# Kernel optimization log

Measured on AMD Instinct MI355X. Metric: run time of the kernel, lower is better.

The kernel has to match this reference:

```python
import jax, jax.numpy as jnp
import numpy as np

EPS = 0.001
FLOW_WARP_WEIGHT = 1.0
_GRAY_W = jnp.array([0.299, 0.587, 0.114], dtype=jnp.float32)


def _to_gray(img):
    # img: [B, 3, H, W] -> [B, 1, H, W] luminance
    return jnp.einsum('bchw,c->bhw', img, _GRAY_W.astype(img.dtype))[:, None]


def _resize_bilinear_align_corners(x, h_out, w_out):
    # x: [B, C, H, W] -> [B, C, h_out, w_out], bilinear, align_corners=True
    B, C, H, W = x.shape
    sy = jnp.arange(h_out, dtype=x.dtype) * ((H - 1) / max(h_out - 1, 1))
    sx = jnp.arange(w_out, dtype=x.dtype) * ((W - 1) / max(w_out - 1, 1))
    y0 = jnp.floor(sy).astype(jnp.int32)
    x0 = jnp.floor(sx).astype(jnp.int32)
    y1 = jnp.minimum(y0 + 1, H - 1)
    x1 = jnp.minimum(x0 + 1, W - 1)
    wy = (sy - y0)[:, None]            # [h_out, 1]
    wx = (sx - x0)[None, :]            # [1, w_out]
    # interp along H
    xh = x[:, :, y0, :] * (1.0 - wy)[..., None].squeeze(-1)[None, None] if False else x[:, :, y0, :] * (1.0 - wy) + x[:, :, y1, :] * wy  # [B,C,h_out,W]
    # interp along W
    out = xh[:, :, :, x0] * (1.0 - wx) + xh[:, :, :, x1] * wx
    return out


def _resize_flow_to_image(flow, h_img, w_img):
    flow_uv = flow[:, :2]
    fh, fw = flow_uv.shape[-2:]
    if (fh, fw) == (h_img, w_img):
        return flow_uv
    r = _resize_bilinear_align_corners(flow_uv, h_img, w_img)
    scale = jnp.array([w_img / max(fw, 1), h_img / max(fh, 1)], dtype=flow.dtype)
    return r * scale[None, :, None, None]


def _bilinear_sample_zeros(img, gx, gy):
    # img: [B, 1, H, W]; gx, gy: [B, H, W] pixel coords (align_corners=True)
    B, _, H, W = img.shape
    x0f = jnp.floor(gx)
    y0f = jnp.floor(gy)
    wx = gx - x0f
    wy = gy - y0f
    x0 = x0f.astype(jnp.int32)
    y0 = y0f.astype(jnp.int32)
    b = jnp.arange(B)[:, None, None]

    def gather(yi, xi):
        valid = (xi >= 0) & (xi <= W - 1) & (yi >= 0) & (yi <= H - 1)
        v = img[b, 0, jnp.clip(yi, 0, H - 1), jnp.clip(xi, 0, W - 1)]
        return jnp.where(valid, v, jnp.zeros((), img.dtype))

    v00 = gather(y0, x0)
    v01 = gather(y0, x0 + 1)
    v10 = gather(y0 + 1, x0)
    v11 = gather(y0 + 1, x0 + 1)
    out = (v00 * (1 - wx) * (1 - wy) + v01 * wx * (1 - wy)
           + v10 * (1 - wx) * wy + v11 * wx * wy)
    return out[:, None]  # [B,1,H,W]


def _forward(pred_prev, pred_next, flow_prev_to_next):
    prev_g = _to_gray(pred_prev)   # [B,1,H,W]
    next_g = _to_gray(pred_next)
    B, _, H, W = prev_g.shape
    flow_uv = _resize_flow_to_image(flow_prev_to_next, H, W)  # [B,2,H,W]
    yy, xx = jnp.meshgrid(jnp.arange(H, dtype=prev_g.dtype),
                          jnp.arange(W, dtype=prev_g.dtype), indexing='ij')
    gx = xx[None] + flow_uv[:, 0]  # [B,H,W]
    gy = yy[None] + flow_uv[:, 1]
    valid = ((gx >= 0) & (gx <= W - 1) & (gy >= 0) & (gy <= H - 1)).astype(prev_g.dtype)
    warped = _bilinear_sample_zeros(next_g, gx, gy)  # [B,1,H,W]
    diff = prev_g - warped
    valid_mask = valid[:, None]
    valid_count = jnp.maximum(valid_mask.sum(), 1.0)
    loss_map = jnp.sqrt(diff * diff + EPS * EPS) * valid_mask
    loss = loss_map.sum() / valid_count
    return FLOW_WARP_WEIGHT * loss, loss


def setup_inputs() -> dict:
    key = jax.random.key(0)
    k1, k2, k3 = jax.random.split(key, 3)
    pred_prev = jax.random.uniform(k1, (16, 3, 512, 512), dtype=jnp.float32)
    pred_next = jax.random.uniform(k2, (16, 3, 512, 512), dtype=jnp.float32)
    flow = jax.random.normal(k3, (16, 2, 128, 128), dtype=jnp.float32)
    return {"pred_prev": pred_prev, "pred_next": pred_next, "flow_prev_to_next": flow}


def reference(pred_prev, pred_next, flow_prev_to_next):
    return _forward(pred_prev, pred_next, flow_prev_to_next)
```

## Files before the change

### kernel.cpp

```cpp
#include <hip/hip_runtime.h>


typedef _Float16 half8 __attribute__((ext_vector_type(8)));

constexpr int B  = 16;
constexpr int H  = 512;
constexpr int W  = 512;
constexpr int FH = 128;
constexpr int FW = 128;
constexpr int HW  = H * W;
constexpr int IMG = 3 * HW;
constexpr int FHW = FH * FW;
constexpr float EPS = 0.001f;

constexpr int P    = 32;
constexpr int PW   = W + 2 * P;
constexpr int PH   = H + 2 * P;
constexpr int PIMG = PW * PH;
constexpr int PQ8  = PH * (PW / 8);

constexpr int TX = 64, TY = 32;
constexpr int TW = 120, TH = 80;
constexpr int FROWS  = 10;
constexpr int FLOW_F = 2 * FROWS * FW;

constexpr int NB = 2048;

__global__ __launch_bounds__(256) void pad_gray_kernel(
    const float* __restrict__ nxt, _Float16* __restrict__ g)
{
    const int q  = blockIdx.x * 256 + threadIdx.x;
    const int b  = q / PQ8;
    const int r  = q - b * PQ8;
    const int py = r / (PW / 8);
    const int qx = r - py * (PW / 8);
    const int y  = py - P;
    const int xs = qx * 8 - P;
    half8 o = (half8)0;
    if ((unsigned)y < (unsigned)H && (unsigned)xs <= (unsigned)(W - 8)) {
        const float* __restrict__ nb = nxt + (long)b * IMG + y * W + xs;
        #pragma unroll
        for (int h = 0; h < 2; ++h) {
            const float4 rr = *(const float4*)(nb + 4 * h);
            const float4 gg = *(const float4*)(nb + HW + 4 * h);
            const float4 bl = *(const float4*)(nb + 2 * HW + 4 * h);
            o[4 * h + 0] = (_Float16)(0.299f * rr.x + 0.587f * gg.x + 0.114f * bl.x);
            o[4 * h + 1] = (_Float16)(0.299f * rr.y + 0.587f * gg.y + 0.114f * bl.y);
            o[4 * h + 2] = (_Float16)(0.299f * rr.z + 0.587f * gg.z + 0.114f * bl.z);
            o[4 * h + 3] = (_Float16)(0.299f * rr.w + 0.587f * gg.w + 0.114f * bl.w);
        }
    }
    *(half8*)(g + (long)b * PIMG + py * PW + qx * 8) = o;
}

__global__ __launch_bounds__(256) void loss_kernel(
    const float* __restrict__ prev, const _Float16* __restrict__ gpad,
    const float* __restrict__ flow, double* __restrict__ psum,
    unsigned int* __restrict__ pcnt)
{
    __shared__ __align__(16) _Float16 smh[TW * TH];
    __shared__ __align__(16) float    smf[FLOW_F];

    const int bid = ((blockIdx.x & 7) << 8) | (blockIdx.x >> 3);
    const int b   = bid >> 7;
    const int t   = bid & 127;
    const int tx  = t & 7;
    const int ty  = t >> 3;
    const int x0t = tx * TX;
    const int y0t = ty * TY;

    const float fr = (float)(127.0 / 511.0);
    const int fy_lo = (int)((float)y0t * fr);

    const _Float16* __restrict__ gb = gpad + (long)b * PIMG;

    {
        const _Float16* __restrict__ src = gb + (y0t + 8) * PW + (x0t + 8);
        for (int it = threadIdx.x; it < TH * (TW / 8); it += 256) {
            const int r = it / (TW / 8), c = it - r * (TW / 8);
            *(uint4*)(smh + r * TW + c * 8) = *(const uint4*)(src + r * PW + c * 8);
        }
        const float* __restrict__ fsrc = flow + (long)b * 2 * FHW;
        for (int it = threadIdx.x; it < 2 * FROWS * (FW / 4); it += 256) {
            const int c    = it / (FROWS * (FW / 4));
            const int rr   = (it - c * (FROWS * (FW / 4))) >> 5;
            const int c4   = it & 31;
            const int frow = min(fy_lo + rr, FH - 1);
            const float4 v = *(const float4*)(fsrc + c * FHW + frow * FW + c4 * 4);
            *(float4*)(smf + c * (FROWS * FW) + rr * FW + c4 * 4) = v;
        }
    }

    const int xq = threadIdx.x & 15;
    const int yl = threadIdx.x >> 4;
    const int xb = x0t + xq * 4;

    float pg[2][4];
    #pragma unroll
    for (int k = 0; k < 2; ++k) {
        const int y = y0t + yl + k * 16;
        const float* __restrict__ pb = prev + (long)b * IMG + y * W + xb;
        const float4 pr  = *(const float4*)(pb);
        const float4 pgc = *(const float4*)(pb + HW);
        const float4 plc = *(const float4*)(pb + 2 * HW);
        pg[k][0] = 0.299f * pr.x + 0.587f * pgc.x + 0.114f * plc.x;
        pg[k][1] = 0.299f * pr.y + 0.587f * pgc.y + 0.114f * plc.y;
        pg[k][2] = 0.299f * pr.z + 0.587f * pgc.z + 0.114f * plc.z;
        pg[k][3] = 0.299f * pr.w + 0.587f * pgc.w + 0.114f * plc.w;
    }

    __syncthreads();

    const float sxfb = (float)xb * fr;
    const int F  = (int)sxfb;
    const int F2 = min(F + 2, FW - 1);

    double lsum = 0.0;
    unsigned int lcnt = 0;

    #pragma unroll
    for (int k = 0; k < 2; ++k) {
        const int y = y0t + yl + k * 16;

        const float syf = (float)y * fr;
        const int   fy0 = (int)syf;
        const float wy  = syf - (float)fy0;
        const int r0 = fy0 - fy_lo;
        const int r1 = min(fy0 + 1, FH - 1) - fy_lo;

        const float* __restrict__ su = smf;
        const float* __restrict__ sv = smf + FROWS * FW;
        const float u0a = su[r0 * FW + F], u0b = su[r0 * FW + F + 1], u0c = su[r0 * FW + F2];
        const float u1a = su[r1 * FW + F], u1b = su[r1 * FW + F + 1], u1c = su[r1 * FW + F2];
        const float v0a = sv[r0 * FW + F], v0b = sv[r0 * FW + F + 1], v0c = sv[r0 * FW + F2];
        const float v1a = sv[r1 * FW + F], v1b = sv[r1 * FW + F + 1], v1c = sv[r1 * FW + F2];

        #pragma unroll
        for (int i = 0; i < 4; ++i) {
            const int x = xb + i;
            const float sxf = (float)x * fr;
            const int   fx0 = (int)sxf;
            const float wx  = sxf - (float)fx0;
            const int   d   = fx0 - F;

            const float u00 = d ? u0b : u0a, u01 = d ? u0c : u0b;
            const float u10 = d ? u1b : u1a, u11 = d ? u1c : u1b;
            const float v00 = d ? v0b : v0a, v01 = d ? v0c : v0b;
            const float v10 = d ? v1b : v1a, v11 = d ? v1c : v1b;

            const float uc0 = u00 * (1.0f - wy) + u10 * wy;
            const float uc1 = u01 * (1.0f - wy) + u11 * wy;
            const float vc0 = v00 * (1.0f - wy) + v10 * wy;
            const float vc1 = v01 * (1.0f - wy) + v11 * wy;
            const float u = (uc0 * (1.0f - wx) + uc1 * wx) * 4.0f;
            const float v = (vc0 * (1.0f - wx) + vc1 * wx) * 4.0f;

            const float gx = (float)x + u;
            const float gy = (float)y + v;
            const float vm = ((gx >= 0.0f) & (gx <= (float)(W - 1)) &
                              (gy >= 0.0f) & (gy <= (float)(H - 1))) ? 1.0f : 0.0f;

            const float gxf = floorf(gx), gyf = floorf(gy);
            const float wwx = gx - gxf,  wwy = gy - gyf;
            const int ix0 = (int)gxf, iy0 = (int)gyf;

            const int cx = ix0 - (x0t - 24);
            const int ry = iy0 - (y0t - 24);
            float c00, c01, c10, c11;
            if ((unsigned)cx <= (unsigned)(TW - 2) && (unsigned)ry <= (unsigned)(TH - 2)) {
                const int la = ry * TW + cx;
                c00 = (float)smh[la];      c01 = (float)smh[la + 1];
                c10 = (float)smh[la + TW]; c11 = (float)smh[la + TW + 1];
            } else {
                const int iyc = min(max(iy0, -P), PH - P - 2);
                const int ixc = min(max(ix0, -P), PW - P - 2);
                const _Float16* __restrict__ gp = gb + (iyc + P) * PW + (ixc + P);
                c00 = (float)gp[0];  c01 = (float)gp[1];
                c10 = (float)gp[PW]; c11 = (float)gp[PW + 1];
            }

            const float warped = c00 * (1.0f - wwx) * (1.0f - wwy)
                               + c01 * wwx * (1.0f - wwy)
                               + c10 * (1.0f - wwx) * wwy
                               + c11 * wwx * wwy;
            const float diff = pg[k][i] - warped;
            const float l = sqrtf(diff * diff + EPS * EPS);
            lsum += (double)(l * vm);
            lcnt += (unsigned int)vm;
        }
    }

    #pragma unroll
    for (int off = 32; off > 0; off >>= 1) {
        lsum += __shfl_down(lsum, off);
        lcnt += __shfl_down(lcnt, off);
    }
    __shared__ double s_sum[4];
    __shared__ unsigned int s_cnt[4];
    const int wid = threadIdx.x >> 6, lane = threadIdx.x & 63;
    if (lane == 0) { s_sum[wid] = lsum; s_cnt[wid] = lcnt; }
    __syncthreads();
    if (threadIdx.x == 0) {
        psum[blockIdx.x] = s_sum[0] + s_sum[1] + s_sum[2] + s_sum[3];
        pcnt[blockIdx.x] = s_cnt[0] + s_cnt[1] + s_cnt[2] + s_cnt[3];
    }
}

__global__ __launch_bounds__(256) void reduce_kernel(
    const double* __restrict__ psum, const unsigned int* __restrict__ pcnt,
    int nb, float* __restrict__ out)
{
    double s = 0.0;
    unsigned long long c = 0;
    for (int i = threadIdx.x; i < nb; i += 256) {
        s += psum[i];
        c += (unsigned long long)pcnt[i];
    }
    #pragma unroll
    for (int off = 32; off > 0; off >>= 1) {
        s += __shfl_down(s, off);
        c += __shfl_down(c, off);
    }
    __shared__ double ss[4];
    __shared__ unsigned long long sc[4];
    const int wid = threadIdx.x >> 6, lane = threadIdx.x & 63;
    if (lane == 0) { ss[wid] = s; sc[wid] = c; }
    __syncthreads();
    if (threadIdx.x == 0) {
        double ts = ss[0] + ss[1] + ss[2] + ss[3];
        double tc = (double)(sc[0] + sc[1] + sc[2] + sc[3]);
        if (tc < 1.0) tc = 1.0;
        const float loss = (float)(ts / tc);
        out[0] = loss;
        out[1] = loss;
    }
}

__device__ __forceinline__ float gray3(const float* __restrict__ img, int off) {
    return 0.299f * img[off] + 0.587f * img[HW + off] + 0.114f * img[2 * HW + off];
}

__global__ __launch_bounds__(256) void flow_loss_mono_kernel(
    const float* __restrict__ prev, const float* __restrict__ nxt,
    const float* __restrict__ flow, double* __restrict__ psum,
    unsigned int* __restrict__ pcnt)
{
    const int nquad = B * HW / 4;
    const float fr = (float)(127.0 / 511.0);
    double lsum = 0.0;
    unsigned int lcnt = 0;
    for (int q = blockIdx.x * blockDim.x + threadIdx.x; q < nquad;
         q += gridDim.x * blockDim.x) {
        const int pix = q * 4;
        const int b   = pix >> 18;
        const int rem = pix & (HW - 1);
        const int y   = rem >> 9;
        const int x0  = rem & 511;
        const float* __restrict__ pb = prev + (long)b * IMG;
        const float* __restrict__ nb = nxt  + (long)b * IMG;
        const float* __restrict__ fu = flow + (long)b * 2 * FHW;
        const float* __restrict__ fv = fu + FHW;
        const float syf = (float)y * fr;
        const int   fy0 = (int)syf;
        const int   fy1 = min(fy0 + 1, FH - 1);
        const float wy  = syf - (float)fy0;
        #pragma unroll
        for (int i = 0; i < 4; ++i) {
            const int x = x0 + i;
            const float sxf = (float)x * fr;
            const int   fx0 = (int)sxf;
            const int   fx1 = min(fx0 + 1, FW - 1);
            const float wx  = sxf - (float)fx0;
            const float uc0 = fu[fy0 * FW + fx0] * (1.0f - wy) + fu[fy1 * FW + fx0] * wy;
            const float uc1 = fu[fy0 * FW + fx1] * (1.0f - wy) + fu[fy1 * FW + fx1] * wy;
            const float vc0 = fv[fy0 * FW + fx0] * (1.0f - wy) + fv[fy1 * FW + fx0] * wy;
            const float vc1 = fv[fy0 * FW + fx1] * (1.0f - wy) + fv[fy1 * FW + fx1] * wy;
            const float u = (uc0 * (1.0f - wx) + uc1 * wx) * 4.0f;
            const float v = (vc0 * (1.0f - wx) + vc1 * wx) * 4.0f;
            const float gx = (float)x + u;
            const float gy = (float)y + v;
            const float vm = ((gx >= 0.0f) & (gx <= (float)(W - 1)) &
                              (gy >= 0.0f) & (gy <= (float)(H - 1))) ? 1.0f : 0.0f;
            const float gxf = floorf(gx), gyf = floorf(gy);
            const float wwx = gx - gxf, wwy = gy - gyf;
            const int ix0 = (int)gxf, iy0 = (int)gyf;
            const int xc0 = min(max(ix0, 0), W - 1), xc1 = min(max(ix0 + 1, 0), W - 1);
            const int yc0 = min(max(iy0, 0), H - 1), yc1 = min(max(iy0 + 1, 0), H - 1);
            const float okx0 = (ix0 >= 0 && ix0 < W) ? 1.f : 0.f;
            const float okx1 = (ix0 + 1 >= 0 && ix0 + 1 < W) ? 1.f : 0.f;
            const float oky0 = (iy0 >= 0 && iy0 < H) ? 1.f : 0.f;
            const float oky1 = (iy0 + 1 >= 0 && iy0 + 1 < H) ? 1.f : 0.f;
            const float c00 = gray3(nb, yc0 * W + xc0) * oky0 * okx0;
            const float c01 = gray3(nb, yc0 * W + xc1) * oky0 * okx1;
            const float c10 = gray3(nb, yc1 * W + xc0) * oky1 * okx0;
            const float c11 = gray3(nb, yc1 * W + xc1) * oky1 * okx1;
            const float warped = c00 * (1.0f - wwx) * (1.0f - wwy)
                               + c01 * wwx * (1.0f - wwy)
                               + c10 * (1.0f - wwx) * wwy
                               + c11 * wwx * wwy;
            const float pgv = gray3(pb, y * W + x);
            const float diff = pgv - warped;
            const float l = sqrtf(diff * diff + EPS * EPS);
            lsum += (double)(l * vm);
            lcnt += (unsigned int)vm;
        }
    }
    #pragma unroll
    for (int off = 32; off > 0; off >>= 1) {
        lsum += __shfl_down(lsum, off);
        lcnt += __shfl_down(lcnt, off);
    }
    __shared__ double s_sum[4];
    __shared__ unsigned int s_cnt[4];
    const int wid = threadIdx.x >> 6, lane = threadIdx.x & 63;
    if (lane == 0) { s_sum[wid] = lsum; s_cnt[wid] = lcnt; }
    __syncthreads();
    if (threadIdx.x == 0) {
        psum[blockIdx.x] = s_sum[0] + s_sum[1] + s_sum[2] + s_sum[3];
        pcnt[blockIdx.x] = s_cnt[0] + s_cnt[1] + s_cnt[2] + s_cnt[3];
    }
}

extern "C" void kernel_launch(void* const* d_in, const int* in_sizes, int n_in,
                              void* d_out, int out_size, void* d_ws, size_t ws_size,
                              hipStream_t stream) {
    const float* prev = (const float*)d_in[0];
    const float* nxt  = (const float*)d_in[1];
    const float* flow = (const float*)d_in[2];
    float* out = (float*)d_out;

    double* psum = (double*)d_ws;
    unsigned int* pcnt = (unsigned int*)((char*)d_ws + NB * 8);
    const size_t gbuf_off = ((size_t)NB * 12 + 4095) & ~(size_t)4095;
    const size_t pad_bytes = (size_t)B * PIMG * sizeof(_Float16);

    if (ws_size >= gbuf_off + pad_bytes) {
        _Float16* gbuf = (_Float16*)((char*)d_ws + gbuf_off);
        pad_gray_kernel<<<dim3(B * PQ8 / 256), dim3(256), 0, stream>>>(nxt, gbuf);
        loss_kernel<<<dim3(NB), dim3(256), 0, stream>>>(
            prev, gbuf, flow, psum, pcnt);
        reduce_kernel<<<dim3(1), dim3(256), 0, stream>>>(psum, pcnt, NB, out);
    } else {
        flow_loss_mono_kernel<<<dim3(2048), dim3(256), 0, stream>>>(
            prev, nxt, flow, psum, pcnt);
        reduce_kernel<<<dim3(1), dim3(256), 0, stream>>>(psum, pcnt, 2048, out);
    }
}
```

Baseline: 36.67 us.

## Fuse grayscale conversion into loss kernel tile load, drop padded gray buffer

Removes the separate pad_gray kernel and its fp16 padded intermediate. Each loss block now converts its halo tile of the next frame from RGB fp32 to fp16 gray directly into shared memory, and falls back to on-the-fly gray from global memory for out-of-tile samples. This saves a kernel launch and the intermediate write/read. The cost is redundant RGB reads across overlapping halos, three times the bytes per pixel. The workspace-size fallback path is also removed.

Result: slower. 44.02 us (+20.0%).

```diff
diff --git a/kernel.cpp b/kernel.cpp
--- a/kernel.cpp
+++ b/kernel.cpp
@@ -1,7 +1,7 @@
 #include <hip/hip_runtime.h>
 
 
-typedef _Float16 half8 __attribute__((ext_vector_type(8)));
+typedef _Float16 half4v __attribute__((ext_vector_type(4)));
 
 constexpr int B  = 16;
 constexpr int H  = 512;
@@ -13,12 +13,6 @@
 constexpr int FHW = FH * FW;
 constexpr float EPS = 0.001f;
 
-constexpr int P    = 32;
-constexpr int PW   = W + 2 * P;
-constexpr int PH   = H + 2 * P;
-constexpr int PIMG = PW * PH;
-constexpr int PQ8  = PH * (PW / 8);
-
 constexpr int TX = 64, TY = 32;
 constexpr int TW = 120, TH = 80;
 constexpr int FROWS  = 10;
@@ -26,35 +20,12 @@
 
 constexpr int NB = 2048;
 
-__global__ __launch_bounds__(256) void pad_gray_kernel(
-    const float* __restrict__ nxt, _Float16* __restrict__ g)
-{
-    const int q  = blockIdx.x * 256 + threadIdx.x;
-    const int b  = q / PQ8;
-    const int r  = q - b * PQ8;
-    const int py = r / (PW / 8);
-    const int qx = r - py * (PW / 8);
-    const int y  = py - P;
-    const int xs = qx * 8 - P;
-    half8 o = (half8)0;
-    if ((unsigned)y < (unsigned)H && (unsigned)xs <= (unsigned)(W - 8)) {
-        const float* __restrict__ nb = nxt + (long)b * IMG + y * W + xs;
-        #pragma unroll
-        for (int h = 0; h < 2; ++h) {
-            const float4 rr = *(const float4*)(nb + 4 * h);
-            const float4 gg = *(const float4*)(nb + HW + 4 * h);
-            const float4 bl = *(const float4*)(nb + 2 * HW + 4 * h);
-            o[4 * h + 0] = (_Float16)(0.299f * rr.x + 0.587f * gg.x + 0.114f * bl.x);
-            o[4 * h + 1] = (_Float16)(0.299f * rr.y + 0.587f * gg.y + 0.114f * bl.y);
-            o[4 * h + 2] = (_Float16)(0.299f * rr.z + 0.587f * gg.z + 0.114f * bl.z);
-            o[4 * h + 3] = (_Float16)(0.299f * rr.w + 0.587f * gg.w + 0.114f * bl.w);
-        }
-    }
-    *(half8*)(g + (long)b * PIMG + py * PW + qx * 8) = o;
+__device__ __forceinline__ float gray3(const float* __restrict__ img, int off) {
+    return 0.299f * img[off] + 0.587f * img[HW + off] + 0.114f * img[2 * HW + off];
 }
 
 __global__ __launch_bounds__(256) void loss_kernel(
-    const float* __restrict__ prev, const _Float16* __restrict__ gpad,
+    const float* __restrict__ prev, const float* __restrict__ nxt,
     const float* __restrict__ flow, double* __restrict__ psum,
     unsigned int* __restrict__ pcnt)
 {
@@ -72,14 +43,26 @@
     const float fr = (float)(127.0 / 511.0);
     const int fy_lo = (int)((float)y0t * fr);
 
-    const _Float16* __restrict__ gb = gpad + (long)b * PIMG;
-
+    const float* __restrict__ nb = nxt + (long)b * IMG;
+
+    for (int it = threadIdx.x; it < TH * (TW / 4); it += 256) {
+        const int r  = it / (TW / 4), c = it - r * (TW / 4);
+        const int sy = y0t - 24 + r;
+        const int sx = x0t - 24 + c * 4;
+        half4v hv = (half4v)0;
+        if ((unsigned)sy < (unsigned)H && (unsigned)sx <= (unsigned)(W - 4)) {
+            const float* __restrict__ p = nb + sy * W + sx;
+            const float4 rr = *(const float4*)(p);
+            const float4 gg = *(const float4*)(p + HW);
+            const float4 bl = *(const float4*)(p + 2 * HW);
+            hv[0] = (_Float16)(0.299f * rr.x + 0.587f * gg.x + 0.114f * bl.x);
+            hv[1] = (_Float16)(0.299f * rr.y + 0.587f * gg.y + 0.114f * bl.y);
+            hv[2] = (_Float16)(0.299f * rr.z + 0.587f * gg.z + 0.114f * bl.z);
+            hv[3] = (_Float16)(0.299f * rr.w + 0.587f * gg.w + 0.114f * bl.w);
+        }
+        *(half4v*)(smh + r * TW + c * 4) = hv;
+    }
     {
-        const _Float16* __restrict__ src = gb + (y0t + 8) * PW + (x0t + 8);
-        for (int it = threadIdx.x; it < TH * (TW / 8); it += 256) {
-            const int r = it / (TW / 8), c = it - r * (TW / 8);
-            *(uint4*)(smh + r * TW + c * 8) = *(const uint4*)(src + r * PW + c * 8);
-        }
         const float* __restrict__ fsrc = flow + (long)b * 2 * FHW;
         for (int it = threadIdx.x; it < 2 * FROWS * (FW / 4); it += 256) {
             const int c    = it / (FROWS * (FW / 4));
@@ -172,11 +155,16 @@
                 c00 = (float)smh[la];      c01 = (float)smh[la + 1];
                 c10 = (float)smh[la + TW]; c11 = (float)smh[la + TW + 1];
             } else {
-                const int iyc = min(max(iy0, -P), PH - P - 2);
-                const int ixc = min(max(ix0, -P), PW - P - 2);
-                const _Float16* __restrict__ gp = gb + (iyc + P) * PW + (ixc + P);
-                c00 = (float)gp[0];  c01 = (float)gp[1];
-                c10 = (float)gp[PW]; c11 = (float)gp[PW + 1];
+                const bool vx0g = (ix0 >= 0) & (ix0 < W);
+                const bool vx1g = (ix0 + 1 >= 0) & (ix0 + 1 < W);
+                const bool vy0g = (iy0 >= 0) & (iy0 < H);
+                const bool vy1g = (iy0 + 1 >= 0) & (iy0 + 1 < H);
+                const int xc0 = min(max(ix0, 0), W - 1), xc1 = min(max(ix0 + 1, 0), W - 1);
+                const int yc0 = min(max(iy0, 0), H - 1), yc1 = min(max(iy0 + 1, 0), H - 1);
+                c00 = (vy0g & vx0g) ? gray3(nb, yc0 * W + xc0) : 0.0f;
+                c01 = (vy0g & vx1g) ? gray3(nb, yc0 * W + xc1) : 0.0f;
+                c10 = (vy1g & vx0g) ? gray3(nb, yc1 * W + xc0) : 0.0f;
+                c11 = (vy1g & vx1g) ? gray3(nb, yc1 * W + xc1) : 0.0f;
             }
 
             const float warped = c00 * (1.0f - wwx) * (1.0f - wwy)
@@ -236,91 +224,6 @@
     }
 }
 
-__device__ __forceinline__ float gray3(const float* __restrict__ img, int off) {
-    return 0.299f * img[off] + 0.587f * img[HW + off] + 0.114f * img[2 * HW + off];
-}
-
-__global__ __launch_bounds__(256) void flow_loss_mono_kernel(
-    const float* __restrict__ prev, const float* __restrict__ nxt,
-    const float* __restrict__ flow, double* __restrict__ psum,
-    unsigned int* __restrict__ pcnt)
-{
-    const int nquad = B * HW / 4;
-    const float fr = (float)(127.0 / 511.0);
-    double lsum = 0.0;
-    unsigned int lcnt = 0;
-    for (int q = blockIdx.x * blockDim.x + threadIdx.x; q < nquad;
-         q += gridDim.x * blockDim.x) {
-        const int pix = q * 4;
-        const int b   = pix >> 18;
-        const int rem = pix & (HW - 1);
-        const int y   = rem >> 9;
-        const int x0  = rem & 511;
-        const float* __restrict__ pb = prev + (long)b * IMG;
-        const float* __restrict__ nb = nxt  + (long)b * IMG;
-        const float* __restrict__ fu = flow + (long)b * 2 * FHW;
-        const float* __restrict__ fv = fu + FHW;
-        const float syf = (float)y * fr;
-        const int   fy0 = (int)syf;
-        const int   fy1 = min(fy0 + 1, FH - 1);
-        const float wy  = syf - (float)fy0;
-        #pragma unroll
-        for (int i = 0; i < 4; ++i) {
-            const int x = x0 + i;
-            const float sxf = (float)x * fr;
-            const int   fx0 = (int)sxf;
-            const int   fx1 = min(fx0 + 1, FW - 1);
-            const float wx  = sxf - (float)fx0;
-            const float uc0 = fu[fy0 * FW + fx0] * (1.0f - wy) + fu[fy1 * FW + fx0] * wy;
-            const float uc1 = fu[fy0 * FW + fx1] * (1.0f - wy) + fu[fy1 * FW + fx1] * wy;
-            const float vc0 = fv[fy0 * FW + fx0] * (1.0f - wy) + fv[fy1 * FW + fx0] * wy;
-            const float vc1 = fv[fy0 * FW + fx1] * (1.0f - wy) + fv[fy1 * FW + fx1] * wy;
-            const float u = (uc0 * (1.0f - wx) + uc1 * wx) * 4.0f;
-            const float v = (vc0 * (1.0f - wx) + vc1 * wx) * 4.0f;
-            const float gx = (float)x + u;
-            const float gy = (float)y + v;
-            const float vm = ((gx >= 0.0f) & (gx <= (float)(W - 1)) &
-                              (gy >= 0.0f) & (gy <= (float)(H - 1))) ? 1.0f : 0.0f;
-            const float gxf = floorf(gx), gyf = floorf(gy);
-            const float wwx = gx - gxf, wwy = gy - gyf;
-            const int ix0 = (int)gxf, iy0 = (int)gyf;
-            const int xc0 = min(max(ix0, 0), W - 1), xc1 = min(max(ix0 + 1, 0), W - 1);
-            const int yc0 = min(max(iy0, 0), H - 1), yc1 = min(max(iy0 + 1, 0), H - 1);
-            const float okx0 = (ix0 >= 0 && ix0 < W) ? 1.f : 0.f;
-            const float okx1 = (ix0 + 1 >= 0 && ix0 + 1 < W) ? 1.f : 0.f;
-            const float oky0 = (iy0 >= 0 && iy0 < H) ? 1.f : 0.f;
-            const float oky1 = (iy0 + 1 >= 0 && iy0 + 1 < H) ? 1.f : 0.f;
-            const float c00 = gray3(nb, yc0 * W + xc0) * oky0 * okx0;
-            const float c01 = gray3(nb, yc0 * W + xc1) * oky0 * okx1;
-            const float c10 = gray3(nb, yc1 * W + xc0) * oky1 * okx0;
-            const float c11 = gray3(nb, yc1 * W + xc1) * oky1 * okx1;
-            const float warped = c00 * (1.0f - wwx) * (1.0f - wwy)
-                               + c01 * wwx * (1.0f - wwy)
-                               + c10 * (1.0f - wwx) * wwy
-                               + c11 * wwx * wwy;
-            const float pgv = gray3(pb, y * W + x);
-            const float diff = pgv - warped;
-            const float l = sqrtf(diff * diff + EPS * EPS);
-            lsum += (double)(l * vm);
-            lcnt += (unsigned int)vm;
-        }
-    }
-    #pragma unroll
-    for (int off = 32; off > 0; off >>= 1) {
-        lsum += __shfl_down(lsum, off);
-        lcnt += __shfl_down(lcnt, off);
-    }
-    __shared__ double s_sum[4];
-    __shared__ unsigned int s_cnt[4];
-    const int wid = threadIdx.x >> 6, lane = threadIdx.x & 63;
-    if (lane == 0) { s_sum[wid] = lsum; s_cnt[wid] = lcnt; }
-    __syncthreads();
-    if (threadIdx.x == 0) {
-        psum[blockIdx.x] = s_sum[0] + s_sum[1] + s_sum[2] + s_sum[3];
-        pcnt[blockIdx.x] = s_cnt[0] + s_cnt[1] + s_cnt[2] + s_cnt[3];
-    }
-}
-
 extern "C" void kernel_launch(void* const* d_in, const int* in_sizes, int n_in,
                               void* d_out, int out_size, void* d_ws, size_t ws_size,
                               hipStream_t stream) {
@@ -331,18 +234,7 @@
 
     double* psum = (double*)d_ws;
     unsigned int* pcnt = (unsigned int*)((char*)d_ws + NB * 8);
-    const size_t gbuf_off = ((size_t)NB * 12 + 4095) & ~(size_t)4095;
-    const size_t pad_bytes = (size_t)B * PIMG * sizeof(_Float16);
-
-    if (ws_size >= gbuf_off + pad_bytes) {
-        _Float16* gbuf = (_Float16*)((char*)d_ws + gbuf_off);
-        pad_gray_kernel<<<dim3(B * PQ8 / 256), dim3(256), 0, stream>>>(nxt, gbuf);
-        loss_kernel<<<dim3(NB), dim3(256), 0, stream>>>(
-            prev, gbuf, flow, psum, pcnt);
-        reduce_kernel<<<dim3(1), dim3(256), 0, stream>>>(psum, pcnt, NB, out);
-    } else {
-        flow_loss_mono_kernel<<<dim3(2048), dim3(256), 0, stream>>>(
-            prev, nxt, flow, psum, pcnt);
-        reduce_kernel<<<dim3(1), dim3(256), 0, stream>>>(psum, pcnt, 2048, out);
-    }
-}
+
+    loss_kernel<<<dim3(NB), dim3(256), 0, stream>>>(prev, nxt, flow, psum, pcnt);
+    reduce_kernel<<<dim3(1), dim3(256), 0, stream>>>(psum, pcnt, NB, out);
+}
```
